# Kernel tuning notes

Hardware: AMD Instinct MI355X
Metric: run time of the kernel (lower is better)

## Reference

```python
import jax, jax.numpy as jnp
import numpy as np

FOCAL_ALPHA = 0.25
FOCAL_GAMMA = 2.0
EPS_DICE = 1e-6
W = {'segmentation': 1.0, 'dice': 1.0, 'absence': 1.0,
     'attention_supervision': 0.5, 'confidence': 0.1, 'focal_seg': 0.5}

B, S, H, Wd = 8, 8, 512, 512


def setup_inputs() -> dict:
    key = jax.random.key(0)
    k1, k2, k3, k4, k5, k6 = jax.random.split(key, 6)
    seg_logits = jax.random.normal(k1, (B, S, H, Wd), dtype=jnp.float32)
    seg_probs = jax.nn.sigmoid(seg_logits)  # model would produce probs from logits
    seg_targets = (jax.random.uniform(k2, (B, S, H, Wd)) > 0.7).astype(jnp.float32)
    presence_probs = jax.random.uniform(k3, (B, S), dtype=jnp.float32,
                                        minval=1e-4, maxval=1.0 - 1e-4)
    attention_maps = jax.random.uniform(k4, (B, S, H, Wd), dtype=jnp.float32,
                                        minval=1e-4, maxval=1.0 - 1e-4)
    presence_targets = jax.random.randint(k5, (B, S), 0, 2).astype(jnp.int32)
    return {'seg_logits': seg_logits, 'seg_probs': seg_probs,
            'seg_targets': seg_targets, 'presence_probs': presence_probs,
            'attention_maps': attention_maps, 'presence_targets': presence_targets}


def _bce_with_logits(x, t):
    # stable: max(x,0) - x*t + log(1+exp(-|x|)), elementwise
    return jnp.maximum(x, 0.0) - x * t + jnp.log1p(jnp.exp(-jnp.abs(x)))


def _bce_prob(p, t):
    # torch BCELoss clamps log terms at -100
    lp = jnp.clip(jnp.log(p), -100.0)
    lq = jnp.clip(jnp.log1p(-p), -100.0)
    return -(t * lp + (1.0 - t) * lq)


def reference(seg_logits, seg_probs, seg_targets, presence_probs,
              attention_maps, presence_targets):
    pres = presence_targets.astype(jnp.float32)  # [B,S] presence mask
    b, s = pres.shape
    n_cells = float(b * s)

    # per-(b,s) elementwise BCE over spatial dims
    bce = _bce_with_logits(seg_logits, seg_targets)          # [B,S,H,W]
    bce_mean = bce.mean(axis=(-2, -1))                        # [B,S]

    # focal loss per (b,s)
    pt = jnp.exp(-bce)
    focal_mean = (FOCAL_ALPHA * (1.0 - pt) ** FOCAL_GAMMA * bce).mean(axis=(-2, -1))

    # dice per (b,s)
    inter = (seg_probs * seg_targets).sum(axis=(-2, -1))
    denom = seg_probs.sum(axis=(-2, -1)) + seg_targets.sum(axis=(-2, -1))
    dice = 1.0 - (2.0 * inter + EPS_DICE) / (denom + EPS_DICE)  # [B,S]

    cnt = pres.sum()
    safe_cnt = jnp.maximum(cnt, 1.0)

    def masked_avg(x):
        return jnp.where(cnt > 0, (x * pres).sum() / safe_cnt, 0.0)

    seg_loss = masked_avg(bce_mean)
    dice_loss = masked_avg(dice)
    focal_loss = masked_avg(focal_mean)

    # presence (absence) BCE over all (b,s)
    absence_loss = _bce_prob(presence_probs, pres).mean()

    # attention supervision: present-only BCE(attention, seg_target>0.5),
    # summed then divided by B*S (matches original normalization)
    att_target = (seg_targets > 0.5).astype(jnp.float32)
    att_bce_mean = _bce_prob(attention_maps, att_target).mean(axis=(-2, -1))  # [B,S]
    attention_loss = (att_bce_mean * pres).sum() / n_cells

    # confidence penalty: wrong-side-of-0.5 squared margin
    wrong = ((pres == 0.0) & (presence_probs > 0.5)) | \
            ((pres == 1.0) & (presence_probs < 0.5))
    confidence_loss = jnp.where(wrong, (presence_probs - 0.5) ** 2, 0.0).sum() / n_cells

    total = (W['segmentation'] * seg_loss + W['dice'] * dice_loss +
             W['focal_seg'] * focal_loss + W['absence'] * absence_loss +
             W['attention_supervision'] * attention_loss +
             W['confidence'] * confidence_loss)
    return total
```

## Files before the change

kernel.cpp:

```cpp
#include <hip/hip_runtime.h>
#include <hip/hip_bf16.h>
#include <math.h>

#define HW (512 * 512)
#define CELLS 64
#define KCH 32
#define CHUNK (HW / KCH)
#define BLOCK 256

__device__ __forceinline__ void accum4(float4 pv, float4 tv, float4 av,
                                       float& slog, float& sfn, float& si,
                                       float& sp, float& st, float& sa)
{
#pragma unroll
    for (int j = 0; j < 4; ++j) {
        float p = ((const float*)&pv)[j];
        float t = ((const float*)&tv)[j];
        float a = ((const float*)&av)[j];
        bool tpos = (t > 0.5f);

        float pt = tpos ? p : 1.f - p;
        float la = __logf(pt);
        float om = 1.f - pt;

        slog += la;
        sfn  += om * om * la;
        si    = fmaf(p, t, si);
        sp   += p;
        st   += t;

        float aa = tpos ? a : 1.f - a;
        sa += fmaxf(__logf(aa), -100.f);
    }
}

__global__ __launch_bounds__(BLOCK) void partial_kernel(
    const float* __restrict__ pg,
    const float* __restrict__ tg,
    const float* __restrict__ ag,
    float* __restrict__ ws)
{
    const int cell  = blockIdx.x >> 5;
    const int chunk = blockIdx.x & (KCH - 1);
    const size_t base = (size_t)cell * HW + (size_t)chunk * CHUNK;

    const float4* p4 = (const float4*)(pg + base);
    const float4* t4 = (const float4*)(tg + base);
    const float4* a4 = (const float4*)(ag + base);

    float slog = 0.f, sfn = 0.f, si = 0.f, sp = 0.f, st = 0.f, sa = 0.f;

    for (int i = threadIdx.x; i < CHUNK / 4; i += 2 * BLOCK) {
        float4 pv0 = p4[i];
        float4 tv0 = t4[i];
        float4 av0 = a4[i];
        float4 pv1 = p4[i + BLOCK];
        float4 tv1 = t4[i + BLOCK];
        float4 av1 = a4[i + BLOCK];
        accum4(pv0, tv0, av0, slog, sfn, si, sp, st, sa);
        accum4(pv1, tv1, av1, slog, sfn, si, sp, st, sa);
    }

#pragma unroll
    for (int o = 32; o > 0; o >>= 1) {
        slog += __shfl_down(slog, o);
        sfn  += __shfl_down(sfn, o);
        si   += __shfl_down(si, o);
        sp   += __shfl_down(sp, o);
        st   += __shfl_down(st, o);
        sa   += __shfl_down(sa, o);
    }

    __shared__ float red[BLOCK / 64][6];
    const int wave = threadIdx.x >> 6;
    const int lane = threadIdx.x & 63;
    if (lane == 0) {
        red[wave][0] = slog; red[wave][1] = sfn; red[wave][2] = si;
        red[wave][3] = sp;   red[wave][4] = st;  red[wave][5] = sa;
    }
    __syncthreads();
    if (threadIdx.x == 0) {
        float r0 = 0, r1 = 0, r2 = 0, r3 = 0, r4 = 0, r5 = 0;
#pragma unroll
        for (int w = 0; w < BLOCK / 64; ++w) {
            r0 += red[w][0]; r1 += red[w][1]; r2 += red[w][2];
            r3 += red[w][3]; r4 += red[w][4]; r5 += red[w][5];
        }
        float* o = ws + (size_t)blockIdx.x * 8;
        o[0] = -r0;
        o[1] = -r1;
        o[2] = r2;
        o[3] = r3;
        o[4] = r4;
        o[5] = -r5;
    }
}

__global__ __launch_bounds__(64) void finalize_kernel(
    const float* __restrict__ ws,
    const float* __restrict__ presence_probs,
    const int* __restrict__ presence_targets,
    float* __restrict__ out)
{
    const int c = threadIdx.x;

    float sb = 0.f, sf = 0.f, si = 0.f, sp = 0.f, st = 0.f, sa = 0.f;
    const float* w = ws + (size_t)c * KCH * 8;
#pragma unroll 4
    for (int k = 0; k < KCH; ++k) {
        sb += w[0]; sf += w[1]; si += w[2];
        sp += w[3]; st += w[4]; sa += w[5];
        w += 8;
    }

    const float invHW = 1.0f / (float)HW;
    float bce_mean   = sb * invHW;
    float focal_mean = 0.25f * sf * invHW;
    float att_mean   = sa * invHW;
    float dice = 1.f - (2.f * si + 1e-6f) / (sp + st + 1e-6f);

    float pres = (float)presence_targets[c];
    float pp   = presence_probs[c];

    float lp = fmaxf(logf(pp), -100.f);
    float lq = fmaxf(log1pf(-pp), -100.f);
    float absence = -(pres * lp + (1.f - pres) * lq);

    bool wrong = (pres == 0.f && pp > 0.5f) || (pres == 1.f && pp < 0.5f);
    float dm = pp - 0.5f;
    float conf = wrong ? dm * dm : 0.f;

    float cnt = pres;
    float mb = bce_mean * pres;
    float md = dice * pres;
    float mf = focal_mean * pres;
    float ma = att_mean * pres;

#pragma unroll
    for (int o = 32; o > 0; o >>= 1) {
        cnt     += __shfl_down(cnt, o);
        mb      += __shfl_down(mb, o);
        md      += __shfl_down(md, o);
        mf      += __shfl_down(mf, o);
        ma      += __shfl_down(ma, o);
        absence += __shfl_down(absence, o);
        conf    += __shfl_down(conf, o);
    }

    if (threadIdx.x == 0) {
        const float inv_n = 1.0f / (float)CELLS;
        float safe = fmaxf(cnt, 1.f);
        float seg  = (cnt > 0.f) ? mb / safe : 0.f;
        float dce  = (cnt > 0.f) ? md / safe : 0.f;
        float foc  = (cnt > 0.f) ? mf / safe : 0.f;
        float total = 1.0f * seg
                    + 1.0f * dce
                    + 0.5f * foc
                    + 1.0f * (absence * inv_n)
                    + 0.5f * (ma * inv_n)
                    + 0.1f * (conf * inv_n);
        out[0] = total;
    }
}

extern "C" void kernel_launch(void* const* d_in, const int* in_sizes, int n_in,
                              void* d_out, int out_size, void* d_ws, size_t ws_size,
                              hipStream_t stream) {
    const float* seg_probs        = (const float*)d_in[1];
    const float* seg_targets      = (const float*)d_in[2];
    const float* presence_probs   = (const float*)d_in[3];
    const float* attention_maps   = (const float*)d_in[4];
    const int*   presence_targets = (const int*)d_in[5];
    float* ws = (float*)d_ws;

    partial_kernel<<<CELLS * KCH, BLOCK, 0, stream>>>(
        seg_probs, seg_targets, attention_maps, ws);
    finalize_kernel<<<1, 64, 0, stream>>>(
        ws, presence_probs, presence_targets, (float*)d_out);
}
```

Measured before the change: 231.4 us.

## Fuse finalize into main kernel via atomic ticket and prefetch-pipelined grid-stride loads

Merges the partial and finalize kernels into one launch. The last block to finish, chosen with an atomic ticket counter, computes the final loss, and per-cell sums are accumulated with global atomicAdds into a zeroed workspace. The main loop now uses a fixed grid of 1024 blocks with register double-buffering, so the next step's float4 loads are issued before the current step is computed. In exchange it adds a memset, per-step block reductions with two syncthreads per step, and atomic contention on the per-cell accumulators.

Result: slower. 387.8 us (+67.6%).

```diff
diff --git a/kernel.cpp b/kernel.cpp
--- a/kernel.cpp
+++ b/kernel.cpp
@@ -4,9 +4,9 @@
 
 #define HW (512 * 512)
 #define CELLS 64
-#define KCH 32
-#define CHUNK (HW / KCH)
 #define BLOCK 256
+#define GRID 1024
+#define NSTEP 8
 
 __device__ __forceinline__ void accum4(float4 pv, float4 tv, float4 av,
                                        float& slog, float& sfn, float& si,
@@ -34,132 +34,132 @@
     }
 }
 
-__global__ __launch_bounds__(BLOCK) void partial_kernel(
+__global__ __launch_bounds__(BLOCK, 4) void loss_kernel(
     const float* __restrict__ pg,
     const float* __restrict__ tg,
     const float* __restrict__ ag,
-    float* __restrict__ ws)
+    const float* __restrict__ presence_probs,
+    const int* __restrict__ presence_targets,
+    float* __restrict__ ws,
+    float* __restrict__ out)
 {
-    const int cell  = blockIdx.x >> 5;
-    const int chunk = blockIdx.x & (KCH - 1);
-    const size_t base = (size_t)cell * HW + (size_t)chunk * CHUNK;
+    float* acc = ws;
+    unsigned* ticket = (unsigned*)(ws + CELLS * 6);
 
-    const float4* p4 = (const float4*)(pg + base);
-    const float4* t4 = (const float4*)(tg + base);
-    const float4* a4 = (const float4*)(ag + base);
+    __shared__ float red[BLOCK / 64][6];
+    __shared__ unsigned s_ticket;
 
-    float slog = 0.f, sfn = 0.f, si = 0.f, sp = 0.f, st = 0.f, sa = 0.f;
+    const int b    = blockIdx.x;
+    const int wave = threadIdx.x >> 6;
+    const int lane = threadIdx.x & 63;
 
-    for (int i = threadIdx.x; i < CHUNK / 4; i += 2 * BLOCK) {
-        float4 pv0 = p4[i];
-        float4 tv0 = t4[i];
-        float4 av0 = a4[i];
-        float4 pv1 = p4[i + BLOCK];
-        float4 tv1 = t4[i + BLOCK];
-        float4 av1 = a4[i + BLOCK];
-        accum4(pv0, tv0, av0, slog, sfn, si, sp, st, sa);
-        accum4(pv1, tv1, av1, slog, sfn, si, sp, st, sa);
+    float4 Pa, Ta, Aa, Pb, Tb, Ab;
+    {
+        const size_t base = (size_t)b * 2048 + ((size_t)threadIdx.x << 2);
+        Pa = *(const float4*)(pg + base);  Pb = *(const float4*)(pg + base + 1024);
+        Ta = *(const float4*)(tg + base);  Tb = *(const float4*)(tg + base + 1024);
+        Aa = *(const float4*)(ag + base);  Ab = *(const float4*)(ag + base + 1024);
     }
 
+    for (int s = 0; s < NSTEP; ++s) {
+        float4 cPa = Pa, cTa = Ta, cAa = Aa, cPb = Pb, cTb = Tb, cAb = Ab;
+        if (s + 1 < NSTEP) {
+            const size_t nb = ((size_t)(s + 1) * GRID + b) * 2048 +
+                              ((size_t)threadIdx.x << 2);
+            Pa = *(const float4*)(pg + nb);  Pb = *(const float4*)(pg + nb + 1024);
+            Ta = *(const float4*)(tg + nb);  Tb = *(const float4*)(tg + nb + 1024);
+            Aa = *(const float4*)(ag + nb);  Ab = *(const float4*)(ag + nb + 1024);
+        }
+
+        float slog = 0.f, sfn = 0.f, si = 0.f, sp = 0.f, st = 0.f, sa = 0.f;
+        accum4(cPa, cTa, cAa, slog, sfn, si, sp, st, sa);
+        accum4(cPb, cTb, cAb, slog, sfn, si, sp, st, sa);
+
 #pragma unroll
-    for (int o = 32; o > 0; o >>= 1) {
-        slog += __shfl_down(slog, o);
-        sfn  += __shfl_down(sfn, o);
-        si   += __shfl_down(si, o);
-        sp   += __shfl_down(sp, o);
-        st   += __shfl_down(st, o);
-        sa   += __shfl_down(sa, o);
+        for (int o = 32; o > 0; o >>= 1) {
+            slog += __shfl_down(slog, o);
+            sfn  += __shfl_down(sfn, o);
+            si   += __shfl_down(si, o);
+            sp   += __shfl_down(sp, o);
+            st   += __shfl_down(st, o);
+            sa   += __shfl_down(sa, o);
+        }
+        if (lane == 0) {
+            red[wave][0] = slog; red[wave][1] = sfn; red[wave][2] = si;
+            red[wave][3] = sp;   red[wave][4] = st;  red[wave][5] = sa;
+        }
+        __syncthreads();
+        if (threadIdx.x < 6) {
+            const int cell = 8 * s + (b >> 7);
+            float v = red[0][threadIdx.x] + red[1][threadIdx.x] +
+                      red[2][threadIdx.x] + red[3][threadIdx.x];
+            atomicAdd(&acc[cell * 6 + threadIdx.x], v);
+        }
+        __syncthreads();
     }
 
-    __shared__ float red[BLOCK / 64][6];
-    const int wave = threadIdx.x >> 6;
-    const int lane = threadIdx.x & 63;
-    if (lane == 0) {
-        red[wave][0] = slog; red[wave][1] = sfn; red[wave][2] = si;
-        red[wave][3] = sp;   red[wave][4] = st;  red[wave][5] = sa;
-    }
+    __threadfence();
+    if (threadIdx.x == 0) s_ticket = atomicAdd(ticket, 1u);
     __syncthreads();
-    if (threadIdx.x == 0) {
-        float r0 = 0, r1 = 0, r2 = 0, r3 = 0, r4 = 0, r5 = 0;
-#pragma unroll
-        for (int w = 0; w < BLOCK / 64; ++w) {
-            r0 += red[w][0]; r1 += red[w][1]; r2 += red[w][2];
-            r3 += red[w][3]; r4 += red[w][4]; r5 += red[w][5];
-        }
-        float* o = ws + (size_t)blockIdx.x * 8;
-        o[0] = -r0;
-        o[1] = -r1;
-        o[2] = r2;
-        o[3] = r3;
-        o[4] = r4;
-        o[5] = -r5;
-    }
-}
+    if (s_ticket != GRID - 1) return;
 
-__global__ __launch_bounds__(64) void finalize_kernel(
-    const float* __restrict__ ws,
-    const float* __restrict__ presence_probs,
-    const int* __restrict__ presence_targets,
-    float* __restrict__ out)
-{
-    const int c = threadIdx.x;
+    if (threadIdx.x < 64) {
+        const int c = threadIdx.x;
+        float slog = atomicAdd(&acc[c * 6 + 0], 0.f);
+        float sfn  = atomicAdd(&acc[c * 6 + 1], 0.f);
+        float si   = atomicAdd(&acc[c * 6 + 2], 0.f);
+        float sp   = atomicAdd(&acc[c * 6 + 3], 0.f);
+        float st   = atomicAdd(&acc[c * 6 + 4], 0.f);
+        float sa   = atomicAdd(&acc[c * 6 + 5], 0.f);
 
-    float sb = 0.f, sf = 0.f, si = 0.f, sp = 0.f, st = 0.f, sa = 0.f;
-    const float* w = ws + (size_t)c * KCH * 8;
-#pragma unroll 4
-    for (int k = 0; k < KCH; ++k) {
-        sb += w[0]; sf += w[1]; si += w[2];
-        sp += w[3]; st += w[4]; sa += w[5];
-        w += 8;
-    }
+        const float invHW = 1.0f / (float)HW;
+        float bce_mean   = -slog * invHW;
+        float focal_mean = 0.25f * -sfn * invHW;
+        float att_mean   = -sa * invHW;
+        float dice = 1.f - (2.f * si + 1e-6f) / (sp + st + 1e-6f);
 
-    const float invHW = 1.0f / (float)HW;
-    float bce_mean   = sb * invHW;
-    float focal_mean = 0.25f * sf * invHW;
-    float att_mean   = sa * invHW;
-    float dice = 1.f - (2.f * si + 1e-6f) / (sp + st + 1e-6f);
+        float pres = (float)presence_targets[c];
+        float pp   = presence_probs[c];
 
-    float pres = (float)presence_targets[c];
-    float pp   = presence_probs[c];
+        float lp = fmaxf(logf(pp), -100.f);
+        float lq = fmaxf(log1pf(-pp), -100.f);
+        float absence = -(pres * lp + (1.f - pres) * lq);
 
-    float lp = fmaxf(logf(pp), -100.f);
-    float lq = fmaxf(log1pf(-pp), -100.f);
-    float absence = -(pres * lp + (1.f - pres) * lq);
+        bool wrong = (pres == 0.f && pp > 0.5f) || (pres == 1.f && pp < 0.5f);
+        float dm = pp - 0.5f;
+        float conf = wrong ? dm * dm : 0.f;
 
-    bool wrong = (pres == 0.f && pp > 0.5f) || (pres == 1.f && pp < 0.5f);
-    float dm = pp - 0.5f;
-    float conf = wrong ? dm * dm : 0.f;
-
-    float cnt = pres;
-    float mb = bce_mean * pres;
-    float md = dice * pres;
-    float mf = focal_mean * pres;
-    float ma = att_mean * pres;
+        float cnt = pres;
+        float mb = bce_mean * pres;
+        float md = dice * pres;
+        float mf = focal_mean * pres;
+        float ma = att_mean * pres;
 
 #pragma unroll
-    for (int o = 32; o > 0; o >>= 1) {
-        cnt     += __shfl_down(cnt, o);
-        mb      += __shfl_down(mb, o);
-        md      += __shfl_down(md, o);
-        mf      += __shfl_down(mf, o);
-        ma      += __shfl_down(ma, o);
-        absence += __shfl_down(absence, o);
-        conf    += __shfl_down(conf, o);
-    }
+        for (int o = 32; o > 0; o >>= 1) {
+            cnt     += __shfl_down(cnt, o);
+            mb      += __shfl_down(mb, o);
+            md      += __shfl_down(md, o);
+            mf      += __shfl_down(mf, o);
+            ma      += __shfl_down(ma, o);
+            absence += __shfl_down(absence, o);
+            conf    += __shfl_down(conf, o);
+        }
 
-    if (threadIdx.x == 0) {
-        const float inv_n = 1.0f / (float)CELLS;
-        float safe = fmaxf(cnt, 1.f);
-        float seg  = (cnt > 0.f) ? mb / safe : 0.f;
-        float dce  = (cnt > 0.f) ? md / safe : 0.f;
-        float foc  = (cnt > 0.f) ? mf / safe : 0.f;
-        float total = 1.0f * seg
-                    + 1.0f * dce
-                    + 0.5f * foc
-                    + 1.0f * (absence * inv_n)
-                    + 0.5f * (ma * inv_n)
-                    + 0.1f * (conf * inv_n);
-        out[0] = total;
+        if (threadIdx.x == 0) {
+            const float inv_n = 1.0f / (float)CELLS;
+            float safe = fmaxf(cnt, 1.f);
+            float seg  = (cnt > 0.f) ? mb / safe : 0.f;
+            float dce  = (cnt > 0.f) ? md / safe : 0.f;
+            float foc  = (cnt > 0.f) ? mf / safe : 0.f;
+            float total = 1.0f * seg
+                        + 1.0f * dce
+                        + 0.5f * foc
+                        + 1.0f * (absence * inv_n)
+                        + 0.5f * (ma * inv_n)
+                        + 0.1f * (conf * inv_n);
+            out[0] = total;
+        }
     }
 }
 
@@ -173,8 +173,9 @@
     const int*   presence_targets = (const int*)d_in[5];
     float* ws = (float*)d_ws;
 
-    partial_kernel<<<CELLS * KCH, BLOCK, 0, stream>>>(
-        seg_probs, seg_targets, attention_maps, ws);
-    finalize_kernel<<<1, 64, 0, stream>>>(
-        ws, presence_probs, presence_targets, (float*)d_out);
+    hipMemsetAsync(ws, 0, (CELLS * 6 + 1) * sizeof(float), stream);
+
+    loss_kernel<<<GRID, BLOCK, 0, stream>>>(
+        seg_probs, seg_targets, attention_maps,
+        presence_probs, presence_targets, ws, (float*)d_out);
 }
```

## Stage inputs through LDS with async global_load_lds double buffering

Applied to the files above, without the earlier changes.

Replaces direct float4 global loads with asynchronous global-to-LDS copies into a double-buffered shared tile, and halves the grid to 1024 blocks, each covering a larger chunk. The goal is to overlap memory fetch for the next tile with compute on the current one. It adds two block barriers per iteration and LDS traffic, and each thread now processes only one float4 per iteration instead of two. The finalize kernel still reads KCH partials per cell, and KCH is now derived from the new grid, so the two kernels stay consistent.

After: 232.4 us. Within noise of the previous version (+0.4%).

```diff
diff --git a/kernel.cpp b/kernel.cpp
--- a/kernel.cpp
+++ b/kernel.cpp
@@ -4,9 +4,11 @@
 
 #define HW (512 * 512)
 #define CELLS 64
-#define KCH 32
+#define BLOCK 256
+#define GRID 1024
+#define KCH (GRID / CELLS)
 #define CHUNK (HW / KCH)
-#define BLOCK 256
+#define ITERS (CHUNK / 1024)
 
 __device__ __forceinline__ void accum4(float4 pv, float4 tv, float4 av,
                                        float& slog, float& sfn, float& si,
@@ -32,6 +34,13 @@
         float aa = tpos ? a : 1.f - a;
         sa += fmaxf(__logf(aa), -100.f);
     }
+}
+
+__device__ __forceinline__ void stage16(const float* g, float* lds) {
+    __builtin_amdgcn_global_load_lds(
+        (const __attribute__((address_space(1))) unsigned int*)g,
+        (__attribute__((address_space(3))) unsigned int*)lds,
+        16, 0, 0);
 }
 
 __global__ __launch_bounds__(BLOCK) void partial_kernel(
@@ -40,25 +49,42 @@
     const float* __restrict__ ag,
     float* __restrict__ ws)
 {
-    const int cell  = blockIdx.x >> 5;
-    const int chunk = blockIdx.x & (KCH - 1);
-    const size_t base = (size_t)cell * HW + (size_t)chunk * CHUNK;
-
-    const float4* p4 = (const float4*)(pg + base);
-    const float4* t4 = (const float4*)(tg + base);
-    const float4* a4 = (const float4*)(ag + base);
+    __shared__ float sb[2][3][1024];
+
+    const int tid  = threadIdx.x;
+    const int wv   = tid >> 6;
+    const int lane = tid & 63;
+
+    const int cell = blockIdx.x >> 4;
+    const int sub  = blockIdx.x & (KCH - 1);
+    const size_t base = (size_t)cell * HW + (size_t)sub * CHUNK;
+
+    const float* p0 = pg + base;
+    const float* t0 = tg + base;
+    const float* a0 = ag + base;
+
+    auto stageAll = [&](int buf, int it) {
+        const size_t off = (size_t)it * 1024 + (size_t)tid * 4;
+        float* dst = &sb[buf][0][wv * 256];
+        stage16(p0 + off, dst);
+        stage16(t0 + off, dst + 1024);
+        stage16(a0 + off, dst + 2048);
+    };
 
     float slog = 0.f, sfn = 0.f, si = 0.f, sp = 0.f, st = 0.f, sa = 0.f;
 
-    for (int i = threadIdx.x; i < CHUNK / 4; i += 2 * BLOCK) {
-        float4 pv0 = p4[i];
-        float4 tv0 = t4[i];
-        float4 av0 = a4[i];
-        float4 pv1 = p4[i + BLOCK];
-        float4 tv1 = t4[i + BLOCK];
-        float4 av1 = a4[i + BLOCK];
-        accum4(pv0, tv0, av0, slog, sfn, si, sp, st, sa);
-        accum4(pv1, tv1, av1, slog, sfn, si, sp, st, sa);
+    stageAll(0, 0);
+    for (int it = 0; it < ITERS; ++it) {
+        const int cur = it & 1;
+        if (it + 1 < ITERS) stageAll(cur ^ 1, it + 1);
+        __syncthreads();
+
+        float4 pv = *(const float4*)&sb[cur][0][tid * 4];
+        float4 tv = *(const float4*)&sb[cur][1][tid * 4];
+        float4 av = *(const float4*)&sb[cur][2][tid * 4];
+        accum4(pv, tv, av, slog, sfn, si, sp, st, sa);
+
+        __syncthreads();
     }
 
 #pragma unroll
@@ -72,14 +98,12 @@
     }
 
     __shared__ float red[BLOCK / 64][6];
-    const int wave = threadIdx.x >> 6;
-    const int lane = threadIdx.x & 63;
     if (lane == 0) {
-        red[wave][0] = slog; red[wave][1] = sfn; red[wave][2] = si;
-        red[wave][3] = sp;   red[wave][4] = st;  red[wave][5] = sa;
+        red[wv][0] = slog; red[wv][1] = sfn; red[wv][2] = si;
+        red[wv][3] = sp;   red[wv][4] = st;  red[wv][5] = sa;
     }
     __syncthreads();
-    if (threadIdx.x == 0) {
+    if (tid == 0) {
         float r0 = 0, r1 = 0, r2 = 0, r3 = 0, r4 = 0, r5 = 0;
 #pragma unroll
         for (int w = 0; w < BLOCK / 64; ++w) {
@@ -173,7 +197,7 @@
     const int*   presence_targets = (const int*)d_in[5];
     float* ws = (float*)d_ws;
 
-    partial_kernel<<<CELLS * KCH, BLOCK, 0, stream>>>(
+    partial_kernel<<<GRID, BLOCK, 0, stream>>>(
         seg_probs, seg_targets, attention_maps, ws);
     finalize_kernel<<<1, 64, 0, stream>>>(
         ws, presence_probs, presence_targets, (float*)d_out);
```
